# Performance work log

Measured on AMD Instinct MI355X. Metric: run time of the kernel, lower is better.

The kernel has to match this reference:

```python
import jax, jax.numpy as jnp
import numpy as np

N = 100000   # nodes
E = 1600000  # edges (self-loop free by construction)
B = 512      # graphs in batch
F = 128      # input node features
HID = 128    # hidden dim
HEADS = 4
CH = HID // HEADS  # 32
EPS_BN = 1e-5


def setup_inputs() -> dict:
    key = jax.random.key(0)
    ks = jax.random.split(key, 24)
    x = jax.random.normal(ks[0], (N, F), jnp.float32)
    dst = jax.random.randint(ks[1], (E,), 0, N)
    off = jax.random.randint(ks[2], (E,), 1, N)
    src = (dst + off) % N  # guaranteed no self loops
    edge_index = jnp.stack([src, dst]).astype(jnp.int32)
    batch = jnp.sort(jax.random.randint(ks[3], (N,), 0, B)).astype(jnp.int32)
    g = lambda k, shape, fan: jax.random.normal(k, shape, jnp.float32) / np.sqrt(fan)
    return {
        "x": x, "edge_index": edge_index, "batch": batch,
        "W_in": g(ks[4], (F, HID), F), "b_in": jnp.zeros((HID,), jnp.float32),
        "lin_w": g(ks[5], (2, HID, HID), HID),
        "att_src": g(ks[6], (2, HEADS, CH), CH),
        "att_dst": g(ks[7], (2, HEADS, CH), CH),
        "conv_b": jnp.zeros((2, HID), jnp.float32),
        "lin_w_last": g(ks[8], (HID, HID), HID),
        "att_src_last": g(ks[9], (HID,), HID),
        "att_dst_last": g(ks[10], (HID,), HID),
        "b_last": jnp.zeros((HID,), jnp.float32),
        "bn_g": jnp.ones((3, HID), jnp.float32) + 0.1 * jax.random.normal(ks[11], (3, HID), jnp.float32),
        "bn_b": 0.1 * jax.random.normal(ks[12], (3, HID), jnp.float32),
        "bn_m": 0.1 * jax.random.normal(ks[13], (3, HID), jnp.float32),
        "bn_v": 0.5 + jax.random.uniform(ks[14], (3, HID), jnp.float32),
        "ro_w1": g(ks[15], (HID, HID // 2), HID),
        "ro_b1": jnp.zeros((HID // 2,), jnp.float32),
        "ro_w2": g(ks[16], (HID // 2, 1), HID // 2),
        "ro_b2": jnp.zeros((1,), jnp.float32),
    }


def _gat_conv(h, src, dst, W, a_src, a_dst, bias, concat):
    """PyG GATConv (shared lin for src/dst, add_self_loops=True, eval mode)."""
    n = h.shape[0]
    heads, ch = a_src.shape
    xs = (h @ W).reshape(n, heads, ch)              # [N,H,C]
    al_s = jnp.sum(xs * a_src, axis=-1)             # [N,H]
    al_d = jnp.sum(xs * a_dst, axis=-1)             # [N,H]
    loop = jnp.arange(n, dtype=src.dtype)
    src_f = jnp.concatenate([src, loop])
    dst_f = jnp.concatenate([dst, loop])
    e = jax.nn.leaky_relu(al_s[src_f] + al_d[dst_f], 0.2)   # [E+N,H]
    m = jax.ops.segment_max(e, dst_f, num_segments=n)       # dest-grouped softmax
    ee = jnp.exp(e - m[dst_f])
    z = jax.ops.segment_sum(ee, dst_f, num_segments=n)
    alpha = ee / (z[dst_f] + 1e-16)                          # [E+N,H]
    out = jax.ops.segment_sum(alpha[:, :, None] * xs[src_f], dst_f, num_segments=n)
    out = out.reshape(n, heads * ch) if concat else jnp.mean(out, axis=1)
    return out + bias


def _bn_eval(h, g, b, m, v):
    return (h - m) * (g / jnp.sqrt(v + EPS_BN)) + b


def _seg_softmax(scores, seg, num_segments):
    m = jax.ops.segment_max(scores, seg, num_segments=num_segments)
    e = jnp.exp(scores - m[seg])
    z = jax.ops.segment_sum(e, seg, num_segments=num_segments)
    return e / z[seg]


def reference(x, edge_index, batch, W_in, b_in, lin_w, att_src, att_dst, conv_b,
              lin_w_last, att_src_last, att_dst_last, b_last,
              bn_g, bn_b, bn_m, bn_v, ro_w1, ro_b1, ro_w2, ro_b2):
    src, dst = edge_index[0], edge_index[1]
    h = x @ W_in + b_in                                       # input_proj
    # first num_layers-1 multi-head concat layers
    for i in range(2):
        h_new = _gat_conv(h, src, dst, lin_w[i], att_src[i], att_dst[i], conv_b[i], True)
        h_new = jax.nn.elu(_bn_eval(h_new, bn_g[i], bn_b[i], bn_m[i], bn_v[i]))
        h = h + h_new                                         # residual (shapes match)
    # final single-head layer, concat=False
    h_new = _gat_conv(h, src, dst, lin_w_last, att_src_last[None, :], att_dst_last[None, :], b_last, False)
    h_new = jax.nn.elu(_bn_eval(h_new, bn_g[2], bn_b[2], bn_m[2], bn_v[2]))
    h = h + h_new
    # attention readout + per-graph softmax over atoms
    atom_scores = (jnp.tanh(h @ ro_w1 + ro_b1) @ ro_w2 + ro_b2)[:, 0]   # [N]
    atom_attention = _seg_softmax(atom_scores, batch, B)
    # attention-weighted add pool
    graph_emb = jax.ops.segment_sum(h * atom_attention[:, None], batch, num_segments=B)
    return graph_emb, atom_attention
```

## Files before the change

### kernel.cpp

```cpp
#include <hip/hip_runtime.h>
#include <math.h>
#include <stdint.h>

#define BSZ 512
#define BSH 9
#define NBKT_MAX 256

typedef __attribute__((ext_vector_type(8))) short bf16x8;
typedef __attribute__((ext_vector_type(4))) float f32x4;

static __device__ __forceinline__ uint32_t f2bf(float x) {
    uint32_t u = __float_as_uint(x);
    return (u + 0x7fffu + ((u >> 16) & 1u)) >> 16;
}
static __device__ __forceinline__ float bflo(uint32_t v) { return __uint_as_float(v << 16); }
static __device__ __forceinline__ float bfhi(uint32_t v) { return __uint_as_float(v & 0xffff0000u); }
static __device__ __forceinline__ void split2(float x, short& hi, short& lo) {
    uint32_t hb = f2bf(x);
    float hf = __uint_as_float(hb << 16);
    uint32_t lb = f2bf(x - hf);
    hi = (short)hb; lo = (short)lb;
}

__global__ void k_binit(int* __restrict__ bcur, int nbkt, int cap) {
    int t = threadIdx.x;
    if (t < nbkt) bcur[t] = t * cap;
}
__global__ __launch_bounds__(256) void k_bucket(const int* __restrict__ src, const int* __restrict__ dst,
                                                int* __restrict__ bcur, uint32_t* __restrict__ bucketed,
                                                int e, int cap) {
    __shared__ int hist[NBKT_MAX];
    __shared__ int cur[NBKT_MAX];
    int t = threadIdx.x;
    hist[t] = 0;
    __syncthreads();
    int base = blockIdx.x * 8192;
#pragma unroll 4
    for (int i = 0; i < 32; ++i) {
        int ei = base + i * 256 + t;
        if (ei < e) atomicAdd(&hist[dst[ei] >> BSH], 1);
    }
    __syncthreads();
    int hc = hist[t];
    cur[t] = (hc > 0) ? atomicAdd(&bcur[t], hc) : 0;
    __syncthreads();
#pragma unroll 4
    for (int i = 0; i < 32; ++i) {
        int ei = base + i * 256 + t;
        if (ei < e) {
            int d = dst[ei], s = src[ei];
            int b = d >> BSH;
            int p = atomicAdd(&cur[b], 1);
            if (p < (b + 1) * cap)
                bucketed[p] = ((uint32_t)(d & (BSZ - 1)) << 23) | (uint32_t)s;
        }
    }
}
__global__ __launch_bounds__(256) void k_bcount(const int* __restrict__ bcur, const uint32_t* __restrict__ bucketed,
                                                int* __restrict__ cnt, int n, int cap) {
    __shared__ int lf[BSZ];
    int b = blockIdx.x, t = threadIdx.x;
    int n0 = b << BSH;
    int nn = min(BSZ, n - n0);
    for (int i = t; i < nn; i += 256) lf[i] = 0;
    __syncthreads();
    int cb = min(bcur[b] - b * cap, cap);
    const uint32_t* ba = bucketed + (size_t)b * cap;
    for (int i = t; i < cb; i += 256) atomicAdd(&lf[ba[i] >> 23], 1);
    __syncthreads();
    for (int i = t; i < nn; i += 256) cnt[n0 + i] = lf[i] + 1;
}
__global__ __launch_bounds__(256) void k_scan1(const int* __restrict__ cnt, int* __restrict__ bsum, int n) {
    __shared__ int sd[256];
    int base = blockIdx.x * 1024, t = threadIdx.x;
    int s = 0;
#pragma unroll
    for (int i = 0; i < 4; ++i) {
        int idx = base + t * 4 + i;
        if (idx < n) s += (cnt[idx] + 3) & ~3;
    }
    sd[t] = s; __syncthreads();
    for (int o = 128; o; o >>= 1) {
        if (t < o) sd[t] += sd[t + o];
        __syncthreads();
    }
    if (t == 0) bsum[blockIdx.x] = sd[0];
}
__global__ void k_scan2(int* __restrict__ bsum, int nb) {
    __shared__ int sd[128];
    int t = threadIdx.x;
    int v = (t < nb) ? bsum[t] : 0;
    sd[t] = v; __syncthreads();
    for (int o = 1; o < 128; o <<= 1) {
        int u = (t >= o) ? sd[t - o] : 0;
        __syncthreads();
        sd[t] += u;
        __syncthreads();
    }
    if (t < nb) bsum[t] = sd[t] - v;
}
__global__ __launch_bounds__(256) void k_scan3(const int* __restrict__ cnt, const int* __restrict__ bsum,
                                               int* __restrict__ rp, int n) {
    __shared__ int sd[256];
    int base = blockIdx.x * 1024, t = threadIdx.x;
    int v[4]; int s = 0;
#pragma unroll
    for (int i = 0; i < 4; ++i) {
        int idx = base + t * 4 + i;
        v[i] = (idx < n) ? ((cnt[idx] + 3) & ~3) : 0;
        s += v[i];
    }
    sd[t] = s; __syncthreads();
    for (int o = 1; o < 256; o <<= 1) {
        int u = (t >= o) ? sd[t - o] : 0;
        __syncthreads();
        sd[t] += u;
        __syncthreads();
    }
    int excl = sd[t] - s + bsum[blockIdx.x];
#pragma unroll
    for (int i = 0; i < 4; ++i) {
        int idx = base + t * 4 + i;
        if (idx < n) rp[idx] = excl;
        excl += v[i];
        if (idx == n - 1) rp[n] = excl;
    }
}
__global__ __launch_bounds__(256) void k_bscatter(const int* __restrict__ bcur, const uint32_t* __restrict__ bucketed,
                                                  const int* __restrict__ rp, int* __restrict__ col,
                                                  int n, int cap) {
    __shared__ int lf[BSZ];
    __shared__ int rpl[BSZ];
    int b = blockIdx.x, t = threadIdx.x;
    int n0 = b << BSH;
    int nn = min(BSZ, n - n0);
    for (int i = t; i < nn; i += 256) {
        int r = rp[n0 + i];
        rpl[i] = r;
        lf[i] = 1;
        col[r] = n0 + i;
    }
    __syncthreads();
    int cb = min(bcur[b] - b * cap, cap);
    const uint32_t* ba = bucketed + (size_t)b * cap;
    for (int i = t; i < cb; i += 256) {
        uint32_t v = ba[i];
        int ld = (int)(v >> 23), s = (int)(v & 0x7fffffu);
        int o = atomicAdd(&lf[ld], 1);
        col[rpl[ld] + o] = s;
    }
    __syncthreads();
    for (int i = t; i < nn; i += 256) {
        int c = lf[i], end = (c + 3) & ~3;
        int r = rpl[i];
        for (int j = c; j < end; ++j) col[r + j] = -1;
    }
}
__global__ void k_bnprep(const float* __restrict__ conv_b, const float* __restrict__ b_last,
                         const float* __restrict__ bn_g, const float* __restrict__ bn_b,
                         const float* __restrict__ bn_m, const float* __restrict__ bn_v,
                         float* __restrict__ sc, float* __restrict__ sh) {
    int i = blockIdx.x * 128 + threadIdx.x;
    if (i >= 384) return;
    int layer = i >> 7, c = i & 127;
    float bias = (layer < 2) ? conv_b[layer * 128 + c] : b_last[c];
    float s = bn_g[i] * __frsqrt_rn(bn_v[i] + 1e-5f);
    sc[i] = s;
    sh[i] = (bias - bn_m[i]) * s + bn_b[i];
}
__global__ __launch_bounds__(256) void k_wprep(const float* __restrict__ W_in, const float* __restrict__ lin_w,
                                               const float* __restrict__ lin_w_last,
                                               uint16_t* __restrict__ wfh, uint16_t* __restrict__ wfl) {
    int i = blockIdx.x * 256 + threadIdx.x;
    int m = i >> 14, e = i & 16383;
    const float* src = (m == 0) ? W_in : (m == 1) ? lin_w : (m == 2) ? (lin_w + 16384) : lin_w_last;
    float v = src[e];
    int k = e >> 7, n = e & 127;
    int kc = k >> 5, g = (k >> 3) & 3, j = k & 7, ct = n >> 4, cln = n & 15;
    int idx = m * 16384 + (((kc * 8 + ct) * 64) + g * 16 + cln) * 8 + j;
    short hi, lo;
    split2(v, hi, lo);
    wfh[idx] = hi; wfl[idx] = lo;
}

template <int ATT, int OBF>
__global__ __launch_bounds__(256) void k_gemm(
    const float* __restrict__ A, const uint16_t* __restrict__ wfh, const uint16_t* __restrict__ wfl,
    const float* __restrict__ bias, void* __restrict__ outv,
    const float* __restrict__ atts, const float* __restrict__ attd,
    float* __restrict__ als, float* __restrict__ ald, int nrows)
{
    __shared__ __align__(16) char smem[65536];
    const int t = threadIdx.x;
    const int l = t & 63, wv = t >> 6;
    const int cl = l & 15, gl = l >> 4;
    const int row0w = blockIdx.x * 128 + wv * 32;

    {
        const uint4* gh = (const uint4*)wfh;
        const uint4* glo = (const uint4*)wfl;
        uint4* sh = (uint4*)smem;
        uint4* sl = (uint4*)(smem + 32768);
#pragma unroll
        for (int i = 0; i < 8; ++i) {
            sh[t + i * 256] = gh[t + i * 256];
            sl[t + i * 256] = glo[t + i * 256];
        }
    }

    float bloc[8], avsl[8], avdl[8];
    if (ATT == 0) {
#pragma unroll
        for (int ct = 0; ct < 8; ++ct) bloc[ct] = bias[ct * 16 + cl];
    } else {
#pragma unroll
        for (int ct = 0; ct < 8; ++ct) { avsl[ct] = atts[ct * 16 + cl]; avdl[ct] = attd[ct * 16 + cl]; }
    }

    bf16x8 Ah[2][4], Al[2][4];
#pragma unroll
    for (int rt = 0; rt < 2; ++rt) {
        int row = row0w + rt * 16 + cl;
        bool ok = row < nrows;
        const float* ap = A + (size_t)row * 128 + gl * 8;
#pragma unroll
        for (int kc = 0; kc < 4; ++kc) {
            float4 u = make_float4(0.f, 0.f, 0.f, 0.f), v = u;
            if (ok) {
                u = *(const float4*)(ap + kc * 32);
                v = *(const float4*)(ap + kc * 32 + 4);
            }
            float xv[8] = {u.x, u.y, u.z, u.w, v.x, v.y, v.z, v.w};
            bf16x8 hbv, lbv;
#pragma unroll
            for (int j = 0; j < 8; ++j) {
                short hi, lo;
                split2(xv[j], hi, lo);
                hbv[j] = hi; lbv[j] = lo;
            }
            Ah[rt][kc] = hbv; Al[rt][kc] = lbv;
        }
    }
    __syncthreads();

    const uint16_t* WH = (const uint16_t*)smem;
    const uint16_t* WL = (const uint16_t*)(smem + 32768);
    f32x4 acc[2][8];
#pragma unroll
    for (int rt = 0; rt < 2; ++rt)
#pragma unroll
        for (int ct = 0; ct < 8; ++ct) { f32x4 z = {0.f, 0.f, 0.f, 0.f}; acc[rt][ct] = z; }
#pragma unroll
    for (int kc = 0; kc < 4; ++kc) {
        bf16x8 bh[8], bl[8];
#pragma unroll
        for (int ct = 0; ct < 8; ++ct) {
            bh[ct] = *(const bf16x8*)&WH[(((kc * 8 + ct) * 64) + l) * 8];
            bl[ct] = *(const bf16x8*)&WL[(((kc * 8 + ct) * 64) + l) * 8];
        }
#pragma unroll
        for (int rt = 0; rt < 2; ++rt)
#pragma unroll
            for (int ct = 0; ct < 8; ++ct) {
                acc[rt][ct] = __builtin_amdgcn_mfma_f32_16x16x32_bf16(Ah[rt][kc], bh[ct], acc[rt][ct], 0, 0, 0);
                acc[rt][ct] = __builtin_amdgcn_mfma_f32_16x16x32_bf16(Ah[rt][kc], bl[ct], acc[rt][ct], 0, 0, 0);
                acc[rt][ct] = __builtin_amdgcn_mfma_f32_16x16x32_bf16(Al[rt][kc], bh[ct], acc[rt][ct], 0, 0, 0);
            }
    }
    __syncthreads();

    if (OBF) {
        uint16_t* out = (uint16_t*)outv;
        uint16_t* buf = (uint16_t*)(smem + wv * 16384);
#pragma unroll
        for (int rt = 0; rt < 2; ++rt) {
#pragma unroll
            for (int ct = 0; ct < 8; ++ct)
#pragma unroll
                for (int r = 0; r < 4; ++r)
                    buf[(gl * 4 + r) * 152 + ct * 16 + cl] = (uint16_t)f2bf(acc[rt][ct][r]);
#pragma unroll
            for (int ri = 0; ri < 4; ++ri) {
                int rloc = ri * 4 + gl;
                int row = row0w + rt * 16 + rloc;
                if (row < nrows) {
                    uint4 v = *(const uint4*)&buf[rloc * 152 + cl * 8];
                    *(uint4*)&out[(size_t)row * 128 + cl * 8] = v;
                }
            }
        }
    } else {
        float* out = (float*)outv;
        float* buf = (float*)(smem + wv * 16384);
#pragma unroll
        for (int rt = 0; rt < 2; ++rt) {
#pragma unroll
            for (int ct = 0; ct < 8; ++ct)
#pragma unroll
                for (int r = 0; r < 4; ++r)
                    buf[(gl * 4 + r) * 136 + ct * 16 + cl] = acc[rt][ct][r] + bloc[ct];
#pragma unroll
            for (int ri = 0; ri < 4; ++ri) {
                int rloc = ri * 4 + gl;
                int row = row0w + rt * 16 + rloc;
                if (row < nrows) {
                    float4 v0 = *(const float4*)&buf[rloc * 136 + cl * 8];
                    float4 v1 = *(const float4*)&buf[rloc * 136 + cl * 8 + 4];
                    *(float4*)&out[(size_t)row * 128 + cl * 8] = v0;
                    *(float4*)&out[(size_t)row * 128 + cl * 8 + 4] = v1;
                }
            }
        }
    }

    if (ATT == 4) {
#pragma unroll
        for (int rt = 0; rt < 2; ++rt)
#pragma unroll
            for (int r = 0; r < 4; ++r) {
                float s[4], d[4];
#pragma unroll
                for (int hh = 0; hh < 4; ++hh) {
                    s[hh] = acc[rt][2 * hh][r] * avsl[2 * hh] + acc[rt][2 * hh + 1][r] * avsl[2 * hh + 1];
                    d[hh] = acc[rt][2 * hh][r] * avdl[2 * hh] + acc[rt][2 * hh + 1][r] * avdl[2 * hh + 1];
                }
#pragma unroll
                for (int hh = 0; hh < 4; ++hh) {
                    s[hh] += __shfl_xor(s[hh], 1); s[hh] += __shfl_xor(s[hh], 2);
                    s[hh] += __shfl_xor(s[hh], 4); s[hh] += __shfl_xor(s[hh], 8);
                    d[hh] += __shfl_xor(d[hh], 1); d[hh] += __shfl_xor(d[hh], 2);
                    d[hh] += __shfl_xor(d[hh], 4); d[hh] += __shfl_xor(d[hh], 8);
                }
                int row = row0w + rt * 16 + gl * 4 + r;
                if (row < nrows && cl < 4) { als[row * 4 + cl] = s[cl]; ald[row * 4 + cl] = d[cl]; }
            }
    } else if (ATT == 1) {
#pragma unroll
        for (int rt = 0; rt < 2; ++rt)
#pragma unroll
            for (int r = 0; r < 4; ++r) {
                float s = 0.f, d = 0.f;
#pragma unroll
                for (int ct = 0; ct < 8; ++ct) {
                    s += acc[rt][ct][r] * avsl[ct];
                    d += acc[rt][ct][r] * avdl[ct];
                }
                s += __shfl_xor(s, 1); s += __shfl_xor(s, 2); s += __shfl_xor(s, 4); s += __shfl_xor(s, 8);
                d += __shfl_xor(d, 1); d += __shfl_xor(d, 2); d += __shfl_xor(d, 4); d += __shfl_xor(d, 8);
                int row = row0w + rt * 16 + gl * 4 + r;
                if (row < nrows && cl == 0) { als[row] = s; ald[row] = d; }
            }
    }
}

template <int H>
__global__ __launch_bounds__(256) void k_agg(
    const int* __restrict__ rp, const int* __restrict__ col,
    const float* __restrict__ als, const float* __restrict__ ald_,
    const uint16_t* __restrict__ xs, const float* __restrict__ bnsc,
    const float* __restrict__ bnsh, float* __restrict__ h, int n)
{
    constexpr int EPG = (H == 4) ? 16 : 64;
    int node = blockIdx.x * 4 + (threadIdx.x >> 6);
    if (node >= n) return;
    int l = threadIdx.x & 63;
    int hl = (H == 4) ? (l >> 4) : 0;
    int lbase = (H == 4) ? (l & 48) : 0;
    int c0 = l * 2;
    float ad = ald_[node * H + hl];
    int jb = rp[node], je = rp[node + 1];
    float2 hv = *(const float2*)&h[(size_t)node * 128 + c0];
    float sc0v = bnsc[c0], sc1v = bnsc[c0 + 1];
    float sh0v = bnsh[c0], sh1v = bnsh[c0 + 1];

    float z = 0.f, a0 = 0.f, a1 = 0.f;
    for (int j = jb; j < je; j += EPG) {
        int e_l = j + (l & (EPG - 1));
        int s_l = (e_l < je) ? col[e_l] : -1;
        int t_l = s_l < 0 ? 0 : s_l;
        float lg = ((H == 4) ? als[t_l * 4 + hl] : als[t_l]) + ad;
        lg = fmaxf(lg, 0.2f * lg);
        float p_l = (s_l < 0) ? 0.f : __expf(lg);
        int ng = min(EPG, je - j);
        int q = 0;
        for (; q + 8 <= ng; q += 8) {
            int4 ca = *(const int4*)&col[j + q];
            int4 cb = *(const int4*)&col[j + q + 4];
            float p0 = __shfl(p_l, lbase | (q + 0));
            float p1 = __shfl(p_l, lbase | (q + 1));
            float p2 = __shfl(p_l, lbase | (q + 2));
            float p3 = __shfl(p_l, lbase | (q + 3));
            float p4 = __shfl(p_l, lbase | (q + 4));
            float p5 = __shfl(p_l, lbase | (q + 5));
            float p6 = __shfl(p_l, lbase | (q + 6));
            float p7 = __shfl(p_l, lbase | (q + 7));
            int t0 = max(ca.x, 0), t1 = max(ca.y, 0), t2 = max(ca.z, 0), t3 = max(ca.w, 0);
            int t4 = max(cb.x, 0), t5 = max(cb.y, 0), t6 = max(cb.z, 0), t7 = max(cb.w, 0);
            uint32_t x0 = *(const uint32_t*)(xs + (size_t)t0 * 128 + c0);
            uint32_t x1 = *(const uint32_t*)(xs + (size_t)t1 * 128 + c0);
            uint32_t x2 = *(const uint32_t*)(xs + (size_t)t2 * 128 + c0);
            uint32_t x3 = *(const uint32_t*)(xs + (size_t)t3 * 128 + c0);
            uint32_t x4 = *(const uint32_t*)(xs + (size_t)t4 * 128 + c0);
            uint32_t x5 = *(const uint32_t*)(xs + (size_t)t5 * 128 + c0);
            uint32_t x6 = *(const uint32_t*)(xs + (size_t)t6 * 128 + c0);
            uint32_t x7 = *(const uint32_t*)(xs + (size_t)t7 * 128 + c0);
            z += ((p0 + p1) + (p2 + p3)) + ((p4 + p5) + (p6 + p7));
            float s0 = fmaf(p0, bflo(x0), fmaf(p1, bflo(x1), fmaf(p2, bflo(x2), p3 * bflo(x3))));
            float s1 = fmaf(p4, bflo(x4), fmaf(p5, bflo(x5), fmaf(p6, bflo(x6), p7 * bflo(x7))));
            a0 += s0 + s1;
            float u0 = fmaf(p0, bfhi(x0), fmaf(p1, bfhi(x1), fmaf(p2, bfhi(x2), p3 * bfhi(x3))));
            float u1 = fmaf(p4, bfhi(x4), fmaf(p5, bfhi(x5), fmaf(p6, bfhi(x6), p7 * bfhi(x7))));
            a1 += u0 + u1;
        }
        if (q < ng) {
            int4 ca = *(const int4*)&col[j + q];
            float p0 = __shfl(p_l, lbase | (q + 0));
            float p1 = __shfl(p_l, lbase | (q + 1));
            float p2 = __shfl(p_l, lbase | (q + 2));
            float p3 = __shfl(p_l, lbase | (q + 3));
            int t0 = max(ca.x, 0), t1 = max(ca.y, 0), t2 = max(ca.z, 0), t3 = max(ca.w, 0);
            uint32_t x0 = *(const uint32_t*)(xs + (size_t)t0 * 128 + c0);
            uint32_t x1 = *(const uint32_t*)(xs + (size_t)t1 * 128 + c0);
            uint32_t x2 = *(const uint32_t*)(xs + (size_t)t2 * 128 + c0);
            uint32_t x3 = *(const uint32_t*)(xs + (size_t)t3 * 128 + c0);
            z += (p0 + p1) + (p2 + p3);
            a0 = fmaf(p0, bflo(x0), fmaf(p1, bflo(x1), fmaf(p2, bflo(x2), fmaf(p3, bflo(x3), a0))));
            a1 = fmaf(p0, bfhi(x0), fmaf(p1, bfhi(x1), fmaf(p2, bfhi(x2), fmaf(p3, bfhi(x3), a1))));
        }
    }
    float inv = 1.f / z;
    float y0 = fmaf(a0 * inv, sc0v, sh0v);
    float y1 = fmaf(a1 * inv, sc1v, sh1v);
    y0 = y0 > 0.f ? y0 : expm1f(y0);
    y1 = y1 > 0.f ? y1 : expm1f(y1);
    hv.x += y0; hv.y += y1;
    *(float2*)&h[(size_t)node * 128 + c0] = hv;
}

__global__ __launch_bounds__(256) void k_scores(
    const float* __restrict__ h, const float* __restrict__ w1, const float* __restrict__ b1,
    const float* __restrict__ w2, const float* __restrict__ b2,
    float* __restrict__ scores, int n)
{
    __shared__ float W1s[128 * 64];
    __shared__ float As[16][132];
    __shared__ float red[4][32][4];
    const int t = threadIdx.x;
    {
        const float4* w4 = (const float4*)w1;
        float4* s4 = (float4*)W1s;
#pragma unroll
        for (int i = 0; i < 8; ++i) s4[t + i * 256] = w4[t + i * 256];
    }
    const int rg = t & 31, cg = t >> 5;
    const int r0 = rg * 4, c0 = cg * 8;
    const int row0 = blockIdx.x * 128;
    const int ar = (t * 2) >> 2;
    const int ak0 = ((t * 2) & 3) * 4, ak1 = ((t * 2 + 1) & 3) * 4;
    float bloc[8], w2loc[8];
#pragma unroll
    for (int j = 0; j < 8; ++j) { bloc[j] = b1[c0 + j]; w2loc[j] = w2[c0 + j]; }

    float acc[4][8] = {};
    for (int kc = 0; kc < 8; ++kc) {
        __syncthreads();
        {
            float4 v0 = make_float4(0.f, 0.f, 0.f, 0.f), v1 = v0;
            int row = row0 + ar;
            if (row < n) {
                v0 = *(const float4*)&h[(size_t)row * 128 + kc * 16 + ak0];
                v1 = *(const float4*)&h[(size_t)row * 128 + kc * 16 + ak1];
            }
            As[ak0 + 0][ar] = v0.x; As[ak0 + 1][ar] = v0.y; As[ak0 + 2][ar] = v0.z; As[ak0 + 3][ar] = v0.w;
            As[ak1 + 0][ar] = v1.x; As[ak1 + 1][ar] = v1.y; As[ak1 + 2][ar] = v1.z; As[ak1 + 3][ar] = v1.w;
        }
        __syncthreads();
#pragma unroll
        for (int kk = 0; kk < 16; ++kk) {
            float a[4], w[8];
            *(float4*)&a[0] = *(const float4*)&As[kk][r0];
            *(float4*)&w[0] = *(const float4*)&W1s[(kc * 16 + kk) * 64 + c0];
            *(float4*)&w[4] = *(const float4*)&W1s[(kc * 16 + kk) * 64 + c0 + 4];
#pragma unroll
            for (int r = 0; r < 4; ++r)
#pragma unroll
                for (int j = 0; j < 8; ++j) acc[r][j] += a[r] * w[j];
        }
    }
    float part[4];
#pragma unroll
    for (int r = 0; r < 4; ++r) {
        float s = 0.f;
#pragma unroll
        for (int j = 0; j < 8; ++j) s += tanhf(acc[r][j] + bloc[j]) * w2loc[j];
        part[r] = s;
    }
#pragma unroll
    for (int r = 0; r < 4; ++r) part[r] += __shfl_xor(part[r], 32);
    const int wv = t >> 6;
    if ((t & 32) == 0) {
#pragma unroll
        for (int r = 0; r < 4; ++r) red[wv][rg][r] = part[r];
    }
    __syncthreads();
    if (t < 128) {
        int row = row0 + t;
        if (row < n) {
            float s = red[0][t >> 2][t & 3] + red[1][t >> 2][t & 3]
                    + red[2][t >> 2][t & 3] + red[3][t >> 2][t & 3];
            scores[row] = s + b2[0];
        }
    }
}
__global__ void k_graph_ptr(const int* __restrict__ batch, int* __restrict__ gptr, int n, int B) {
    int i = blockIdx.x * 256 + threadIdx.x;
    if (i >= n) return;
    int b = batch[i];
    int bp = (i == 0) ? -1 : batch[i - 1];
    for (int g = bp + 1; g <= b; ++g) gptr[g] = i;
    if (i == n - 1)
        for (int g = b + 1; g <= B; ++g) gptr[g] = n;
}
__global__ __launch_bounds__(256) void k_graph_mz(const int* __restrict__ gptr, const float* __restrict__ scores,
                                                  float* __restrict__ gmax, float* __restrict__ gz, int B) {
    int g = blockIdx.x * 4 + (threadIdx.x >> 6);
    if (g >= B) return;
    int l = threadIdx.x & 63;
    int s0 = gptr[g], s1 = gptr[g + 1];
    float m = -INFINITY;
    for (int i = s0 + l; i < s1; i += 64) m = fmaxf(m, scores[i]);
#pragma unroll
    for (int off = 32; off; off >>= 1) m = fmaxf(m, __shfl_xor(m, off));
    float z = 0.f;
    for (int i = s0 + l; i < s1; i += 64) z += __expf(scores[i] - m);
#pragma unroll
    for (int off = 32; off; off >>= 1) z += __shfl_xor(z, off);
    if (l == 0) { gmax[g] = m; gz[g] = z; }
}
__global__ void k_att(const int* __restrict__ batch, const float* __restrict__ scores,
                      const float* __restrict__ gmax, const float* __restrict__ gz,
                      float* __restrict__ att, int n) {
    int i = blockIdx.x * 256 + threadIdx.x;
    if (i >= n) return;
    int b = batch[i];
    att[i] = __expf(scores[i] - gmax[b]) / gz[b];
}
__global__ __launch_bounds__(256) void k_emb(const int* __restrict__ gptr, const float* __restrict__ att,
                                             const float* __restrict__ h, float* __restrict__ emb) {
    __shared__ float sd[16][64];
    int g = blockIdx.x >> 1, half = blockIdx.x & 1;
    int t = threadIdx.x;
    int cq = (t & 15) * 4;
    int c = half * 64 + cq;
    int p = t >> 4;
    int s0 = gptr[g], s1 = gptr[g + 1];
    float4 acc = make_float4(0.f, 0.f, 0.f, 0.f);
    for (int i = s0 + p; i < s1; i += 16) {
        float a = att[i];
        float4 hvv = *(const float4*)&h[(size_t)i * 128 + c];
        acc.x += a * hvv.x; acc.y += a * hvv.y; acc.z += a * hvv.z; acc.w += a * hvv.w;
    }
    *(float4*)&sd[p][cq] = acc;
    __syncthreads();
    if (t < 64) {
        float s = 0.f;
#pragma unroll
        for (int q = 0; q < 16; ++q) s += sd[q][t];
        emb[g * 128 + half * 64 + t] = s;
    }
}

extern "C" void kernel_launch(void* const* d_in, const int* in_sizes, int n_in,
                              void* d_out, int out_size, void* d_ws, size_t ws_size,
                              hipStream_t stream)
{
    const float* x            = (const float*)d_in[0];
    const int*   eidx         = (const int*)d_in[1];
    const int*   batch        = (const int*)d_in[2];
    const float* W_in         = (const float*)d_in[3];
    const float* b_in         = (const float*)d_in[4];
    const float* lin_w        = (const float*)d_in[5];
    const float* att_src      = (const float*)d_in[6];
    const float* att_dst      = (const float*)d_in[7];
    const float* conv_b       = (const float*)d_in[8];
    const float* lin_w_last   = (const float*)d_in[9];
    const float* att_src_last = (const float*)d_in[10];
    const float* att_dst_last = (const float*)d_in[11];
    const float* b_last       = (const float*)d_in[12];
    const float* bn_g         = (const float*)d_in[13];
    const float* bn_b         = (const float*)d_in[14];
    const float* bn_m         = (const float*)d_in[15];
    const float* bn_v         = (const float*)d_in[16];
    const float* ro_w1        = (const float*)d_in[17];
    const float* ro_b1        = (const float*)d_in[18];
    const float* ro_w2        = (const float*)d_in[19];
    const float* ro_b2        = (const float*)d_in[20];

    const int N = in_sizes[0] / 128;
    const int E = in_sizes[1] / 2;
    const int B = 512;
    const int* esrc = eidx;
    const int* edst = eidx + E;
    const int colcap = E + 4 * N + 64;
    const int NBKT = (N + BSZ - 1) >> BSH;
    const int cap = (E / NBKT) * 3 / 2 + 512;

    char* wsp = (char*)d_ws;
    size_t off = 0;
    auto alloc = [&](size_t bytes) -> void* {
        void* p = wsp + off;
        off += (bytes + 511) & ~(size_t)511;
        return p;
    };
    float*    h      = (float*)alloc((size_t)N * 128 * 4);
    uint16_t* xs     = (uint16_t*)alloc((size_t)N * 128 * 2);
    float*    als    = (float*)alloc((size_t)N * 4 * 4);
    float*    ald    = (float*)alloc((size_t)N * 4 * 4);
    float*    scores = (float*)alloc((size_t)N * 4);
    int*      rp     = (int*)alloc((size_t)(N + 1) * 4);
    int*      col    = (int*)alloc((size_t)colcap * 4);
    int*      cnt    = (int*)alloc((size_t)N * 4);
    int*      bsum   = (int*)alloc(4096);
    int*      gptr   = (int*)alloc((size_t)(B + 1) * 4);
    float*    gmax   = (float*)alloc((size_t)B * 4);
    float*    gz     = (float*)alloc((size_t)B * 4);
    float*    bnsc   = (float*)alloc(384 * 4);
    float*    bnsh   = (float*)alloc(384 * 4);
    int*      bcur   = (int*)alloc(NBKT_MAX * 4);
    uint16_t* wfh    = (uint16_t*)alloc(4 * 16384 * 2);
    uint16_t* wfl    = (uint16_t*)alloc(4 * 16384 * 2);
    uint32_t* bucketed = (uint32_t*)alloc((size_t)NBKT * cap * 4);
    (void)ws_size; (void)n_in; (void)out_size;

    float* emb = (float*)d_out;
    float* att = (float*)d_out + (size_t)B * 128;

    const int nb = (N + 1023) / 1024;
    hipLaunchKernelGGL(k_binit, dim3(1), dim3(256), 0, stream, bcur, NBKT, cap);
    hipLaunchKernelGGL(k_bucket, dim3((E + 8191) / 8192), dim3(256), 0, stream,
                       esrc, edst, bcur, bucketed, E, cap);
    hipLaunchKernelGGL(k_bcount, dim3(NBKT), dim3(256), 0, stream, bcur, bucketed, cnt, N, cap);
    hipLaunchKernelGGL(k_scan1, dim3(nb), dim3(256), 0, stream, cnt, bsum, N);
    hipLaunchKernelGGL(k_scan2, dim3(1), dim3(128), 0, stream, bsum, nb);
    hipLaunchKernelGGL(k_scan3, dim3(nb), dim3(256), 0, stream, cnt, bsum, rp, N);
    hipLaunchKernelGGL(k_bscatter, dim3(NBKT), dim3(256), 0, stream, bcur, bucketed, rp, col, N, cap);
    hipLaunchKernelGGL(k_bnprep, dim3(3), dim3(128), 0, stream, conv_b, b_last, bn_g, bn_b, bn_m, bn_v, bnsc, bnsh);
    hipLaunchKernelGGL(k_wprep, dim3(256), dim3(256), 0, stream, W_in, lin_w, lin_w_last, wfh, wfl);

    const int ntiles = (N + 127) / 128;
    hipLaunchKernelGGL((k_gemm<0, 0>), dim3(ntiles), dim3(256), 0, stream,
                       x, wfh, wfl, b_in, (void*)h, (const float*)nullptr, (const float*)nullptr,
                       (float*)nullptr, (float*)nullptr, N);
    for (int i = 0; i < 2; ++i) {
        hipLaunchKernelGGL((k_gemm<4, 1>), dim3(ntiles), dim3(256), 0, stream,
                           h, wfh + (size_t)(i + 1) * 16384, wfl + (size_t)(i + 1) * 16384,
                           (const float*)nullptr, (void*)xs,
                           att_src + i * 128, att_dst + i * 128, als, ald, N);
        hipLaunchKernelGGL((k_agg<4>), dim3((N + 3) / 4), dim3(256), 0, stream,
                           rp, col, als, ald, xs, bnsc + i * 128, bnsh + i * 128, h, N);
    }
    hipLaunchKernelGGL((k_gemm<1, 1>), dim3(ntiles), dim3(256), 0, stream,
                       h, wfh + (size_t)3 * 16384, wfl + (size_t)3 * 16384,
                       (const float*)nullptr, (void*)xs,
                       att_src_last, att_dst_last, als, ald, N);
    hipLaunchKernelGGL((k_agg<1>), dim3((N + 3) / 4), dim3(256), 0, stream,
                       rp, col, als, ald, xs, bnsc + 256, bnsh + 256, h, N);

    hipLaunchKernelGGL(k_scores, dim3(ntiles), dim3(256), 0, stream,
                       h, ro_w1, ro_b1, ro_w2, ro_b2, scores, N);
    hipLaunchKernelGGL(k_graph_ptr, dim3((N + 255) / 256), dim3(256), 0, stream, batch, gptr, N, B);
    hipLaunchKernelGGL(k_graph_mz, dim3((B + 3) / 4), dim3(256), 0, stream, gptr, scores, gmax, gz, B);
    hipLaunchKernelGGL(k_att, dim3((N + 255) / 256), dim3(256), 0, stream, batch, scores, gmax, gz, att, N);
    hipLaunchKernelGGL(k_emb, dim3(B * 2), dim3(256), 0, stream, gptr, att, h, emb);
}
```

Before: 491.9 us.

## Shrink GEMM tiles for occupancy and fuse readout softmax and pooling

The projection GEMM now processes 64 rows per block instead of 128. It stages only the high bf16 weight half in shared memory (36 KB instead of 64 KB) and reads the low half directly from global memory, with launch bounds requesting 3 blocks per CU to raise occupancy. Separately, the per-graph max/normalizer, attention, and embedding kernels are merged into one per-graph readout kernel. That kernel skips the max subtraction, which relies on the readout scores being bounded so the exponentials cannot overflow. The trade-offs are more global or L1 traffic for the low weights, less register reuse across row tiles, and reduced numerical headroom in the softmax.

```diff
diff --git a/kernel.cpp b/kernel.cpp
--- a/kernel.cpp
+++ b/kernel.cpp
@@ -184,28 +184,23 @@
 }
 
 template <int ATT, int OBF>
-__global__ __launch_bounds__(256) void k_gemm(
+__global__ __launch_bounds__(256, 3) void k_gemm(
     const float* __restrict__ A, const uint16_t* __restrict__ wfh, const uint16_t* __restrict__ wfl,
     const float* __restrict__ bias, void* __restrict__ outv,
     const float* __restrict__ atts, const float* __restrict__ attd,
     float* __restrict__ als, float* __restrict__ ald, int nrows)
 {
-    __shared__ __align__(16) char smem[65536];
+    __shared__ __align__(16) char smem[36864];
     const int t = threadIdx.x;
     const int l = t & 63, wv = t >> 6;
     const int cl = l & 15, gl = l >> 4;
-    const int row0w = blockIdx.x * 128 + wv * 32;
+    const int row0w = blockIdx.x * 64 + wv * 16;
 
     {
         const uint4* gh = (const uint4*)wfh;
-        const uint4* glo = (const uint4*)wfl;
         uint4* sh = (uint4*)smem;
-        uint4* sl = (uint4*)(smem + 32768);
-#pragma unroll
-        for (int i = 0; i < 8; ++i) {
-            sh[t + i * 256] = gh[t + i * 256];
-            sl[t + i * 256] = glo[t + i * 256];
-        }
+#pragma unroll
+        for (int i = 0; i < 8; ++i) sh[t + i * 256] = gh[t + i * 256];
     }
 
     float bloc[8], avsl[8], avdl[8];
@@ -217,10 +212,9 @@
         for (int ct = 0; ct < 8; ++ct) { avsl[ct] = atts[ct * 16 + cl]; avdl[ct] = attd[ct * 16 + cl]; }
     }
 
-    bf16x8 Ah[2][4], Al[2][4];
-#pragma unroll
-    for (int rt = 0; rt < 2; ++rt) {
-        int row = row0w + rt * 16 + cl;
+    bf16x8 Ah[4], Al[4];
+    {
+        int row = row0w + cl;
         bool ok = row < nrows;
         const float* ap = A + (size_t)row * 128 + gl * 8;
 #pragma unroll
@@ -238,118 +232,99 @@
                 split2(xv[j], hi, lo);
                 hbv[j] = hi; lbv[j] = lo;
             }
-            Ah[rt][kc] = hbv; Al[rt][kc] = lbv;
+            Ah[kc] = hbv; Al[kc] = lbv;
         }
     }
     __syncthreads();
 
     const uint16_t* WH = (const uint16_t*)smem;
-    const uint16_t* WL = (const uint16_t*)(smem + 32768);
-    f32x4 acc[2][8];
-#pragma unroll
-    for (int rt = 0; rt < 2; ++rt)
-#pragma unroll
-        for (int ct = 0; ct < 8; ++ct) { f32x4 z = {0.f, 0.f, 0.f, 0.f}; acc[rt][ct] = z; }
+    f32x4 acc[8];
+#pragma unroll
+    for (int ct = 0; ct < 8; ++ct) { f32x4 z = {0.f, 0.f, 0.f, 0.f}; acc[ct] = z; }
 #pragma unroll
     for (int kc = 0; kc < 4; ++kc) {
-        bf16x8 bh[8], bl[8];
 #pragma unroll
         for (int ct = 0; ct < 8; ++ct) {
-            bh[ct] = *(const bf16x8*)&WH[(((kc * 8 + ct) * 64) + l) * 8];
-            bl[ct] = *(const bf16x8*)&WL[(((kc * 8 + ct) * 64) + l) * 8];
-        }
-#pragma unroll
-        for (int rt = 0; rt < 2; ++rt)
-#pragma unroll
-            for (int ct = 0; ct < 8; ++ct) {
-                acc[rt][ct] = __builtin_amdgcn_mfma_f32_16x16x32_bf16(Ah[rt][kc], bh[ct], acc[rt][ct], 0, 0, 0);
-                acc[rt][ct] = __builtin_amdgcn_mfma_f32_16x16x32_bf16(Ah[rt][kc], bl[ct], acc[rt][ct], 0, 0, 0);
-                acc[rt][ct] = __builtin_amdgcn_mfma_f32_16x16x32_bf16(Al[rt][kc], bh[ct], acc[rt][ct], 0, 0, 0);
-            }
+            bf16x8 bh = *(const bf16x8*)&WH[(((kc * 8 + ct) * 64) + l) * 8];
+            bf16x8 bl = *(const bf16x8*)(wfl + (size_t)(((kc * 8 + ct) * 64) + l) * 8);
+            acc[ct] = __builtin_amdgcn_mfma_f32_16x16x32_bf16(Ah[kc], bh, acc[ct], 0, 0, 0);
+            acc[ct] = __builtin_amdgcn_mfma_f32_16x16x32_bf16(Ah[kc], bl, acc[ct], 0, 0, 0);
+            acc[ct] = __builtin_amdgcn_mfma_f32_16x16x32_bf16(Al[kc], bh, acc[ct], 0, 0, 0);
+        }
     }
     __syncthreads();
 
     if (OBF) {
         uint16_t* out = (uint16_t*)outv;
-        uint16_t* buf = (uint16_t*)(smem + wv * 16384);
-#pragma unroll
-        for (int rt = 0; rt < 2; ++rt) {
-#pragma unroll
-            for (int ct = 0; ct < 8; ++ct)
-#pragma unroll
-                for (int r = 0; r < 4; ++r)
-                    buf[(gl * 4 + r) * 152 + ct * 16 + cl] = (uint16_t)f2bf(acc[rt][ct][r]);
-#pragma unroll
-            for (int ri = 0; ri < 4; ++ri) {
-                int rloc = ri * 4 + gl;
-                int row = row0w + rt * 16 + rloc;
-                if (row < nrows) {
-                    uint4 v = *(const uint4*)&buf[rloc * 152 + cl * 8];
-                    *(uint4*)&out[(size_t)row * 128 + cl * 8] = v;
-                }
+        uint16_t* buf = (uint16_t*)(smem + wv * 9216);
+#pragma unroll
+        for (int ct = 0; ct < 8; ++ct)
+#pragma unroll
+            for (int r = 0; r < 4; ++r)
+                buf[(gl * 4 + r) * 152 + ct * 16 + cl] = (uint16_t)f2bf(acc[ct][r]);
+#pragma unroll
+        for (int ri = 0; ri < 4; ++ri) {
+            int rloc = ri * 4 + gl;
+            int row = row0w + rloc;
+            if (row < nrows) {
+                uint4 v = *(const uint4*)&buf[rloc * 152 + cl * 8];
+                *(uint4*)&out[(size_t)row * 128 + cl * 8] = v;
             }
         }
     } else {
         float* out = (float*)outv;
-        float* buf = (float*)(smem + wv * 16384);
-#pragma unroll
-        for (int rt = 0; rt < 2; ++rt) {
-#pragma unroll
-            for (int ct = 0; ct < 8; ++ct)
-#pragma unroll
-                for (int r = 0; r < 4; ++r)
-                    buf[(gl * 4 + r) * 136 + ct * 16 + cl] = acc[rt][ct][r] + bloc[ct];
-#pragma unroll
-            for (int ri = 0; ri < 4; ++ri) {
-                int rloc = ri * 4 + gl;
-                int row = row0w + rt * 16 + rloc;
-                if (row < nrows) {
-                    float4 v0 = *(const float4*)&buf[rloc * 136 + cl * 8];
-                    float4 v1 = *(const float4*)&buf[rloc * 136 + cl * 8 + 4];
-                    *(float4*)&out[(size_t)row * 128 + cl * 8] = v0;
-                    *(float4*)&out[(size_t)row * 128 + cl * 8 + 4] = v1;
-                }
+        float* buf = (float*)(smem + wv * 9216);
+#pragma unroll
+        for (int ct = 0; ct < 8; ++ct)
+#pragma unroll
+            for (int r = 0; r < 4; ++r)
+                buf[(gl * 4 + r) * 136 + ct * 16 + cl] = acc[ct][r] + bloc[ct];
+#pragma unroll
+        for (int ri = 0; ri < 4; ++ri) {
+            int rloc = ri * 4 + gl;
+            int row = row0w + rloc;
+            if (row < nrows) {
+                float4 v0 = *(const float4*)&buf[rloc * 136 + cl * 8];
+                float4 v1 = *(const float4*)&buf[rloc * 136 + cl * 8 + 4];
+                *(float4*)&out[(size_t)row * 128 + cl * 8] = v0;
+                *(float4*)&out[(size_t)row * 128 + cl * 8 + 4] = v1;
             }
         }
     }
 
     if (ATT == 4) {
 #pragma unroll
-        for (int rt = 0; rt < 2; ++rt)
-#pragma unroll
-            for (int r = 0; r < 4; ++r) {
-                float s[4], d[4];
-#pragma unroll
-                for (int hh = 0; hh < 4; ++hh) {
-                    s[hh] = acc[rt][2 * hh][r] * avsl[2 * hh] + acc[rt][2 * hh + 1][r] * avsl[2 * hh + 1];
-                    d[hh] = acc[rt][2 * hh][r] * avdl[2 * hh] + acc[rt][2 * hh + 1][r] * avdl[2 * hh + 1];
-                }
-#pragma unroll
-                for (int hh = 0; hh < 4; ++hh) {
-                    s[hh] += __shfl_xor(s[hh], 1); s[hh] += __shfl_xor(s[hh], 2);
-                    s[hh] += __shfl_xor(s[hh], 4); s[hh] += __shfl_xor(s[hh], 8);
-                    d[hh] += __shfl_xor(d[hh], 1); d[hh] += __shfl_xor(d[hh], 2);
-                    d[hh] += __shfl_xor(d[hh], 4); d[hh] += __shfl_xor(d[hh], 8);
-                }
-                int row = row0w + rt * 16 + gl * 4 + r;
-                if (row < nrows && cl < 4) { als[row * 4 + cl] = s[cl]; ald[row * 4 + cl] = d[cl]; }
-            }
+        for (int r = 0; r < 4; ++r) {
+            float s[4], d[4];
+#pragma unroll
+            for (int hh = 0; hh < 4; ++hh) {
+                s[hh] = acc[2 * hh][r] * avsl[2 * hh] + acc[2 * hh + 1][r] * avsl[2 * hh + 1];
+                d[hh] = acc[2 * hh][r] * avdl[2 * hh] + acc[2 * hh + 1][r] * avdl[2 * hh + 1];
+            }
+#pragma unroll
+            for (int hh = 0; hh < 4; ++hh) {
+                s[hh] += __shfl_xor(s[hh], 1); s[hh] += __shfl_xor(s[hh], 2);
+                s[hh] += __shfl_xor(s[hh], 4); s[hh] += __shfl_xor(s[hh], 8);
+                d[hh] += __shfl_xor(d[hh], 1); d[hh] += __shfl_xor(d[hh], 2);
+                d[hh] += __shfl_xor(d[hh], 4); d[hh] += __shfl_xor(d[hh], 8);
+            }
+            int row = row0w + gl * 4 + r;
+            if (row < nrows && cl < 4) { als[row * 4 + cl] = s[cl]; ald[row * 4 + cl] = d[cl]; }
+        }
     } else if (ATT == 1) {
 #pragma unroll
-        for (int rt = 0; rt < 2; ++rt)
-#pragma unroll
-            for (int r = 0; r < 4; ++r) {
-                float s = 0.f, d = 0.f;
-#pragma unroll
-                for (int ct = 0; ct < 8; ++ct) {
-                    s += acc[rt][ct][r] * avsl[ct];
-                    d += acc[rt][ct][r] * avdl[ct];
-                }
-                s += __shfl_xor(s, 1); s += __shfl_xor(s, 2); s += __shfl_xor(s, 4); s += __shfl_xor(s, 8);
-                d += __shfl_xor(d, 1); d += __shfl_xor(d, 2); d += __shfl_xor(d, 4); d += __shfl_xor(d, 8);
-                int row = row0w + rt * 16 + gl * 4 + r;
-                if (row < nrows && cl == 0) { als[row] = s; ald[row] = d; }
-            }
+        for (int r = 0; r < 4; ++r) {
+            float s = 0.f, d = 0.f;
+#pragma unroll
+            for (int ct = 0; ct < 8; ++ct) {
+                s += acc[ct][r] * avsl[ct];
+                d += acc[ct][r] * avdl[ct];
+            }
+            s += __shfl_xor(s, 1); s += __shfl_xor(s, 2); s += __shfl_xor(s, 4); s += __shfl_xor(s, 8);
+            d += __shfl_xor(d, 1); d += __shfl_xor(d, 2); d += __shfl_xor(d, 4); d += __shfl_xor(d, 8);
+            int row = row0w + gl * 4 + r;
+            if (row < nrows && cl == 0) { als[row] = s; ald[row] = d; }
+        }
     }
 }
 
@@ -521,52 +496,38 @@
     if (i == n - 1)
         for (int g = b + 1; g <= B; ++g) gptr[g] = n;
 }
-__global__ __launch_bounds__(256) void k_graph_mz(const int* __restrict__ gptr, const float* __restrict__ scores,
-                                                  float* __restrict__ gmax, float* __restrict__ gz, int B) {
-    int g = blockIdx.x * 4 + (threadIdx.x >> 6);
-    if (g >= B) return;
-    int l = threadIdx.x & 63;
+__global__ __launch_bounds__(256) void k_readout(const int* __restrict__ gptr, const float* __restrict__ scores,
+                                                 const float* __restrict__ h, float* __restrict__ att,
+                                                 float* __restrict__ emb) {
+    __shared__ float sd[16][128];
+    __shared__ float zred[4];
+    int g = blockIdx.x, t = threadIdx.x;
     int s0 = gptr[g], s1 = gptr[g + 1];
-    float m = -INFINITY;
-    for (int i = s0 + l; i < s1; i += 64) m = fmaxf(m, scores[i]);
-#pragma unroll
-    for (int off = 32; off; off >>= 1) m = fmaxf(m, __shfl_xor(m, off));
-    float z = 0.f;
-    for (int i = s0 + l; i < s1; i += 64) z += __expf(scores[i] - m);
-#pragma unroll
-    for (int off = 32; off; off >>= 1) z += __shfl_xor(z, off);
-    if (l == 0) { gmax[g] = m; gz[g] = z; }
-}
-__global__ void k_att(const int* __restrict__ batch, const float* __restrict__ scores,
-                      const float* __restrict__ gmax, const float* __restrict__ gz,
-                      float* __restrict__ att, int n) {
-    int i = blockIdx.x * 256 + threadIdx.x;
-    if (i >= n) return;
-    int b = batch[i];
-    att[i] = __expf(scores[i] - gmax[b]) / gz[b];
-}
-__global__ __launch_bounds__(256) void k_emb(const int* __restrict__ gptr, const float* __restrict__ att,
-                                             const float* __restrict__ h, float* __restrict__ emb) {
-    __shared__ float sd[16][64];
-    int g = blockIdx.x >> 1, half = blockIdx.x & 1;
-    int t = threadIdx.x;
-    int cq = (t & 15) * 4;
-    int c = half * 64 + cq;
-    int p = t >> 4;
-    int s0 = gptr[g], s1 = gptr[g + 1];
-    float4 acc = make_float4(0.f, 0.f, 0.f, 0.f);
+    float zl = 0.f;
+    for (int i = s0 + t; i < s1; i += 256) zl += __expf(scores[i]);
+#pragma unroll
+    for (int off = 32; off; off >>= 1) zl += __shfl_xor(zl, off);
+    if ((t & 63) == 0) zred[t >> 6] = zl;
+    __syncthreads();
+    float inv = 1.f / (zred[0] + zred[1] + zred[2] + zred[3]);
+    int p = t >> 4, cq = (t & 15) * 8;
+    float4 acc0 = make_float4(0.f, 0.f, 0.f, 0.f), acc1 = acc0;
     for (int i = s0 + p; i < s1; i += 16) {
-        float a = att[i];
-        float4 hvv = *(const float4*)&h[(size_t)i * 128 + c];
-        acc.x += a * hvv.x; acc.y += a * hvv.y; acc.z += a * hvv.z; acc.w += a * hvv.w;
-    }
-    *(float4*)&sd[p][cq] = acc;
-    __syncthreads();
-    if (t < 64) {
+        float a = __expf(scores[i]) * inv;
+        if ((t & 15) == 0) att[i] = a;
+        float4 h0 = *(const float4*)&h[(size_t)i * 128 + cq];
+        float4 h1 = *(const float4*)&h[(size_t)i * 128 + cq + 4];
+        acc0.x += a * h0.x; acc0.y += a * h0.y; acc0.z += a * h0.z; acc0.w += a * h0.w;
+        acc1.x += a * h1.x; acc1.y += a * h1.y; acc1.z += a * h1.z; acc1.w += a * h1.w;
+    }
+    *(float4*)&sd[p][cq] = acc0;
+    *(float4*)&sd[p][cq + 4] = acc1;
+    __syncthreads();
+    if (t < 128) {
         float s = 0.f;
 #pragma unroll
         for (int q = 0; q < 16; ++q) s += sd[q][t];
-        emb[g * 128 + half * 64 + t] = s;
+        emb[g * 128 + t] = s;
     }
 }
 
@@ -622,8 +583,6 @@
     int*      cnt    = (int*)alloc((size_t)N * 4);
     int*      bsum   = (int*)alloc(4096);
     int*      gptr   = (int*)alloc((size_t)(B + 1) * 4);
-    float*    gmax   = (float*)alloc((size_t)B * 4);
-    float*    gz     = (float*)alloc((size_t)B * 4);
     float*    bnsc   = (float*)alloc(384 * 4);
     float*    bnsh   = (float*)alloc(384 * 4);
     int*      bcur   = (int*)alloc(NBKT_MAX * 4);
@@ -647,7 +606,7 @@
     hipLaunchKernelGGL(k_bnprep, dim3(3), dim3(128), 0, stream, conv_b, b_last, bn_g, bn_b, bn_m, bn_v, bnsc, bnsh);
     hipLaunchKernelGGL(k_wprep, dim3(256), dim3(256), 0, stream, W_in, lin_w, lin_w_last, wfh, wfl);
 
-    const int ntiles = (N + 127) / 128;
+    const int ntiles = (N + 63) / 64;
     hipLaunchKernelGGL((k_gemm<0, 0>), dim3(ntiles), dim3(256), 0, stream,
                        x, wfh, wfl, b_in, (void*)h, (const float*)nullptr, (const float*)nullptr,
                        (float*)nullptr, (float*)nullptr, N);
@@ -666,10 +625,8 @@
     hipLaunchKernelGGL((k_agg<1>), dim3((N + 3) / 4), dim3(256), 0, stream,
                        rp, col, als, ald, xs, bnsc + 256, bnsh + 256, h, N);
 
-    hipLaunchKernelGGL(k_scores, dim3(ntiles), dim3(256), 0, stream,
+    hipLaunchKernelGGL(k_scores, dim3((N + 127) / 128), dim3(256), 0, stream,
                        h, ro_w1, ro_b1, ro_w2, ro_b2, scores, N);
     hipLaunchKernelGGL(k_graph_ptr, dim3((N + 255) / 256), dim3(256), 0, stream, batch, gptr, N, B);
-    hipLaunchKernelGGL(k_graph_mz, dim3((B + 3) / 4), dim3(256), 0, stream, gptr, scores, gmax, gz, B);
-    hipLaunchKernelGGL(k_att, dim3((N + 255) / 256), dim3(256), 0, stream, batch, scores, gmax, gz, att, N);
-    hipLaunchKernelGGL(k_emb, dim3(B * 2), dim3(256), 0, stream, gptr, att, h, emb);
-}
+    hipLaunchKernelGGL(k_readout, dim3(B), dim3(256), 0, stream, gptr, scores, h, att, emb);
+}
```

Result: faster. 478.8 us (-2.7%).
